# Performance work log

Measured on AMD Instinct MI355X. Metric: run time of the kernel, lower is better.

Reference implementation:

```python
import jax, jax.numpy as jnp
import numpy as np

N_NODES = 50000
N_EDGES = 1600000
IN_CH = 512
OUT_CH = 512

def setup_inputs() -> dict:
    key = jax.random.key(0)
    k1, k2, k3, k4, k5 = jax.random.split(key, 5)
    x = jax.random.normal(k1, (N_NODES, IN_CH), dtype=jnp.float32)
    adj_vals = jax.random.uniform(k2, (N_EDGES,), dtype=jnp.float32)
    edge_row = jax.random.randint(k3, (N_EDGES,), 0, N_NODES, dtype=jnp.int32)
    edge_col = jax.random.randint(k4, (N_EDGES,), 0, N_NODES, dtype=jnp.int32)
    # weight init per reset_parameters: uniform(-stdv, stdv), stdv = 1/sqrt(out_channel)
    stdv = 1.0 / np.sqrt(OUT_CH)
    weight = jax.random.uniform(k5, (IN_CH, OUT_CH), dtype=jnp.float32,
                                minval=-stdv, maxval=stdv)
    return {"x": x, "adj_vals": adj_vals, "edge_row": edge_row,
            "edge_col": edge_col, "weight": weight}

def reference(x, adj_vals, edge_row, edge_col, weight):
    # support = x @ W  -- dense projection [N, out]
    support = x @ weight
    # output = spmm(adj, support): out[i] = sum_j adj[i, j] * support[j]
    # COO: for edge e = (row, col, val), accumulate val * support[col] into out[row]
    msgs = adj_vals[:, None] * support[edge_col]  # [E, out]
    output = jax.ops.segment_sum(msgs, edge_row, num_segments=N_NODES)
    return output
```

## Files before the change

kernel.cpp:

```cpp
#include <hip/hip_runtime.h>
#include <hip/hip_bf16.h>

#define N_NODES 50000
#define N_EDGES 1600000
#define CH 512
#define M_PAD 50048
#define SCAN_B 196

typedef float f32x4 __attribute__((ext_vector_type(4)));
typedef unsigned short ushort8v __attribute__((ext_vector_type(8)));
typedef _Float16 half8v __attribute__((ext_vector_type(8)));

#define GLOAD_LDS16(gptr, lptr)                                                        \
    __builtin_amdgcn_global_load_lds((const __attribute__((address_space(1))) void*)(gptr), \
                                     (__attribute__((address_space(3))) void*)(lptr), 16, 0, 0)

__device__ inline unsigned short f2h(float x) {
    union { _Float16 h; unsigned short u; } cv;
    cv.h = (_Float16)x;
    return cv.u;
}
__device__ inline float h2f(unsigned short u) {
    union { unsigned short u; _Float16 h; } cv;
    cv.u = u;
    return (float)cv.h;
}


__global__ __launch_bounds__(256) void hist_kernel(const int* __restrict__ row,
                                                   int* __restrict__ counts) {
    int e = blockIdx.x * 256 + threadIdx.x;
    if (e < N_EDGES) atomicAdd(&counts[row[e]], 1);
}

__global__ __launch_bounds__(256) void bsum_kernel(const int* __restrict__ counts,
                                                   int* __restrict__ bsum) {
    __shared__ int red[256];
    int i = blockIdx.x * 256 + threadIdx.x;
    red[threadIdx.x] = (i < N_NODES) ? counts[i] : 0;
    __syncthreads();
    for (int s = 128; s > 0; s >>= 1) {
        if (threadIdx.x < s) red[threadIdx.x] += red[threadIdx.x + s];
        __syncthreads();
    }
    if (threadIdx.x == 0) bsum[blockIdx.x] = red[0];
}

__global__ __launch_bounds__(256) void bscan_kernel(const int* __restrict__ bsum,
                                                    int* __restrict__ bbase) {
    __shared__ int sc[256];
    int t = threadIdx.x;
    int v = (t < SCAN_B) ? bsum[t] : 0;
    sc[t] = v;
    __syncthreads();
    for (int d = 1; d < 256; d <<= 1) {
        int a = (t >= d) ? sc[t - d] : 0;
        __syncthreads();
        sc[t] += a;
        __syncthreads();
    }
    if (t < SCAN_B) bbase[t] = sc[t] - v;
}

__global__ __launch_bounds__(256) void offsets_kernel(const int* __restrict__ counts,
                                                      const int* __restrict__ bbase,
                                                      int* __restrict__ offsets,
                                                      int* __restrict__ nxt) {
    __shared__ int sc[256];
    int t = threadIdx.x;
    int i = blockIdx.x * 256 + t;
    int v = (i < N_NODES) ? counts[i] : 0;
    sc[t] = v;
    __syncthreads();
    for (int d = 1; d < 256; d <<= 1) {
        int a = (t >= d) ? sc[t - d] : 0;
        __syncthreads();
        sc[t] += a;
        __syncthreads();
    }
    int off = bbase[blockIdx.x] + sc[t] - v;
    if (i < N_NODES) { offsets[i] = off; nxt[i] = off; }
    if (i == 0) offsets[N_NODES] = N_EDGES;
}

__global__ __launch_bounds__(256) void scatter_kernel(const int* __restrict__ row,
                                                      const int* __restrict__ col,
                                                      const float* __restrict__ val,
                                                      int* __restrict__ nxt,
                                                      int2* __restrict__ ep) {
    int e = blockIdx.x * 256 + threadIdx.x;
    if (e < N_EDGES) {
        int r = row[e];
        int p = atomicAdd(&nxt[r], 1);
        ep[p] = make_int2(col[e], __float_as_int(val[e]));
    }
}


__global__ __launch_bounds__(256) void prep_x(const float* __restrict__ X,
                                              unsigned short* __restrict__ Xa) {
    const int t = threadIdx.x;
    const int m = blockIdx.x * 32 + (t >> 3);
    const int cpart = t & 7;
    float xv[64];
    if (m < N_NODES) {
        const float* xp = &X[(size_t)m * CH + cpart * 64];
#pragma unroll
        for (int i = 0; i < 16; ++i)
            *(float4*)&xv[i * 4] = *(const float4*)&xp[i * 4];
    } else {
#pragma unroll
        for (int i = 0; i < 64; ++i) xv[i] = 0.f;
    }
#pragma unroll
    for (int kk = 0; kk < 2; ++kk) {
        const int kt = cpart * 2 + kk;
        ushort8v o[4];
#pragma unroll
        for (int q = 0; q < 32; ++q)
            o[q >> 3][q & 7] = f2h(xv[kk * 32 + q]);
        unsigned short* dst = &Xa[((size_t)kt * M_PAD + m) * 32];
        *(ushort8v*)&dst[0]  = o[0];
        *(ushort8v*)&dst[8]  = o[1];
        *(ushort8v*)&dst[16] = o[2];
        *(ushort8v*)&dst[24] = o[3];
    }
}


__global__ __launch_bounds__(256) void prep_w(const float* __restrict__ W,
                                              unsigned short* __restrict__ Wb) {
    __shared__ float tile[32][65];
    const int kt = blockIdx.x;
    const int nb = blockIdx.y * 64;
    const int t = threadIdx.x;
    const int nl = t & 63, kl = t >> 6;
#pragma unroll
    for (int p = 0; p < 8; ++p) {
        int k = p * 4 + kl;
        tile[k][nl] = W[(size_t)(kt * 32 + k) * CH + nb + nl];
    }
    __syncthreads();
    const int n_local = t >> 2, j = t & 3;
    ushort8v hi, lo;
#pragma unroll
    for (int q = 0; q < 8; ++q) {
        float x = tile[j * 8 + q][n_local];
        unsigned short h = f2h(x);
        hi[q] = h;
        lo[q] = f2h(x - h2f(h));
    }
    size_t base = ((size_t)kt * 512 + nb + n_local) * 64 + j * 8;
    *(ushort8v*)&Wb[base] = hi;
    *(ushort8v*)&Wb[base + 32] = lo;
}


__global__ __launch_bounds__(256) void gemm_kernel(const unsigned short* __restrict__ Xa,
                                                   const unsigned short* __restrict__ Wb,
                                                   unsigned short* __restrict__ S) {
    __shared__ __align__(16) unsigned short Al[128 * 32];
    __shared__ __align__(16) unsigned short Bl[128 * 64];

    const int tid = threadIdx.x;
    const int wave = tid >> 6;
    const int lane = tid & 63;
    const int wm = (wave >> 1) * 64;
    const int wn = (wave & 1) * 64;
    const int m0 = blockIdx.x * 128;
    const int n0 = blockIdx.y * 128;

    const int lrow = lane >> 3, lslot = lane & 7;
    const int b_lane_off = lrow * 64 + ((lslot ^ lrow) << 3);
    const int arow_l = lane >> 2, aslot = lane & 3;
    const int a_lane_off = arow_l * 32 + ((aslot ^ (arow_l & 3)) << 3);

    const int fr = lane & 15;
    const int fs = lane >> 4;
    const int fx3 = fr & 3;
    const int fx7 = fr & 7;

    f32x4 acc[4][4] = {};

    for (int kt = 0; kt < 16; ++kt) {
        const unsigned short* bsrc = Wb + ((size_t)kt * 512 + n0 + wave * 32) * 64 + b_lane_off;
        unsigned short* bdst = &Bl[(wave * 32) * 64];
        GLOAD_LDS16(bsrc, bdst);
        GLOAD_LDS16(bsrc + 512, bdst + 512);
        GLOAD_LDS16(bsrc + 1024, bdst + 1024);
        GLOAD_LDS16(bsrc + 1536, bdst + 1536);

        const unsigned short* asrc = Xa + ((size_t)kt * M_PAD + m0 + wave * 16) * 32 + a_lane_off;
        unsigned short* adst = &Al[(wave * 16) * 32];
        GLOAD_LDS16(asrc, adst);
        GLOAD_LDS16(asrc + 64 * 32, adst + 64 * 32);

        __syncthreads();

        half8v af[4];
#pragma unroll
        for (int mi = 0; mi < 4; ++mi)
            af[mi] = *(const half8v*)&Al[(wm + mi * 16 + fr) * 32 + ((fs ^ fx3) << 3)];
#pragma unroll
        for (int ni = 0; ni < 4; ++ni) {
            const unsigned short* br = &Bl[(wn + ni * 16 + fr) * 64];
            half8v bhi = *(const half8v*)&br[((fs ^ fx7) << 3)];
            half8v blo = *(const half8v*)&br[(((fs | 4) ^ fx7) << 3)];
#pragma unroll
            for (int mi = 0; mi < 4; ++mi) {
                acc[mi][ni] = __builtin_amdgcn_mfma_f32_16x16x32_f16(af[mi], bhi, acc[mi][ni], 0, 0, 0);
                acc[mi][ni] = __builtin_amdgcn_mfma_f32_16x16x32_f16(af[mi], blo, acc[mi][ni], 0, 0, 0);
            }
        }
        __syncthreads();
    }

    const int crow = (lane >> 4) * 4;
    const int ccol = lane & 15;
#pragma unroll
    for (int mi = 0; mi < 4; ++mi) {
#pragma unroll
        for (int r = 0; r < 4; ++r) {
            int gm = m0 + wm + mi * 16 + crow + r;
            if (gm < N_NODES) {
#pragma unroll
                for (int ni = 0; ni < 4; ++ni) {
                    S[(size_t)gm * CH + n0 + wn + ni * 16 + ccol] = f2h(acc[mi][ni][r]);
                }
            }
        }
    }
}


__global__ __launch_bounds__(128) void spmm_kernel(const int* __restrict__ offsets,
                                                   const int2* __restrict__ ep,
                                                   const unsigned short* __restrict__ S,
                                                   float* __restrict__ out) {
    const int r = blockIdx.x * 2 + (threadIdx.x >> 6);
    const int lane = threadIdx.x & 63;
    const int c = lane * 8;
    const int start = offsets[r];
    const int end = offsets[r + 1];

    float acc[8] = {0.f, 0.f, 0.f, 0.f, 0.f, 0.f, 0.f, 0.f};
    int e = start;
    for (; e + 3 < end; e += 4) {
        const int2 e0 = ep[e];
        const int2 e1 = ep[e + 1];
        const int2 e2 = ep[e + 2];
        const int2 e3 = ep[e + 3];
        const half8v s0 = *(const half8v*)&S[(size_t)e0.x * CH + c];
        const half8v s1 = *(const half8v*)&S[(size_t)e1.x * CH + c];
        const half8v s2 = *(const half8v*)&S[(size_t)e2.x * CH + c];
        const half8v s3 = *(const half8v*)&S[(size_t)e3.x * CH + c];
        const float v0 = __int_as_float(e0.y);
        const float v1 = __int_as_float(e1.y);
        const float v2 = __int_as_float(e2.y);
        const float v3 = __int_as_float(e3.y);
#pragma unroll
        for (int j = 0; j < 8; ++j) {
            acc[j] += v0 * (float)s0[j];
            acc[j] += v1 * (float)s1[j];
            acc[j] += v2 * (float)s2[j];
            acc[j] += v3 * (float)s3[j];
        }
    }
    for (; e < end; ++e) {
        const int2 e0 = ep[e];
        const half8v s0 = *(const half8v*)&S[(size_t)e0.x * CH + c];
        const float v0 = __int_as_float(e0.y);
#pragma unroll
        for (int j = 0; j < 8; ++j) acc[j] += v0 * (float)s0[j];
    }
    float4 o0 = {acc[0], acc[1], acc[2], acc[3]};
    float4 o1 = {acc[4], acc[5], acc[6], acc[7]};
    *(float4*)&out[(size_t)r * CH + c] = o0;
    *(float4*)&out[(size_t)r * CH + c + 4] = o1;
}


extern "C" void kernel_launch(void* const* d_in, const int* in_sizes, int n_in,
                              void* d_out, int out_size, void* d_ws, size_t ws_size,
                              hipStream_t stream) {
    const float* x        = (const float*)d_in[0];
    const float* adj_vals = (const float*)d_in[1];
    const int*   edge_row = (const int*)d_in[2];
    const int*   edge_col = (const int*)d_in[3];
    const float* weight   = (const float*)d_in[4];
    float* out = (float*)d_out;

    auto align256 = [](size_t v) { return (v + 255) & ~(size_t)255; };
    char* ws = (char*)d_ws;
    size_t off = 0;
    unsigned short* support = (unsigned short*)(ws + off); off = align256(off + (size_t)N_NODES * CH * sizeof(unsigned short));
    unsigned short* Xa = (unsigned short*)(ws + off);      off = align256(off + (size_t)16 * M_PAD * 32 * sizeof(unsigned short));
    int*   counts  = (int*)(ws + off);            off = align256(off + (size_t)N_NODES * sizeof(int));
    int*   offsets = (int*)(ws + off);            off = align256(off + (size_t)(N_NODES + 1) * sizeof(int));
    int*   nxt     = (int*)(ws + off);            off = align256(off + (size_t)N_NODES * sizeof(int));
    int2*  ep      = (int2*)(ws + off);           off = align256(off + (size_t)N_EDGES * sizeof(int2));
    unsigned short* Wb = (unsigned short*)(ws + off); off = align256(off + (size_t)16 * 512 * 64 * sizeof(unsigned short));
    int*   bsum    = (int*)(ws + off);            off = align256(off + (size_t)SCAN_B * sizeof(int));
    int*   bbase   = (int*)(ws + off);            off = align256(off + (size_t)SCAN_B * sizeof(int));

    (void)hipMemsetAsync(counts, 0, (size_t)N_NODES * sizeof(int), stream);

    const int EB = (N_EDGES + 255) / 256;
    hist_kernel<<<EB, 256, 0, stream>>>(edge_row, counts);
    bsum_kernel<<<SCAN_B, 256, 0, stream>>>(counts, bsum);
    bscan_kernel<<<1, 256, 0, stream>>>(bsum, bbase);
    offsets_kernel<<<SCAN_B, 256, 0, stream>>>(counts, bbase, offsets, nxt);
    scatter_kernel<<<EB, 256, 0, stream>>>(edge_row, edge_col, adj_vals, nxt, ep);

    prep_x<<<M_PAD / 32, 256, 0, stream>>>(x, Xa);
    dim3 wgrid(16, 8);
    prep_w<<<wgrid, 256, 0, stream>>>(weight, Wb);

    dim3 ggrid(M_PAD / 128, CH / 128);
    gemm_kernel<<<ggrid, 256, 0, stream>>>(Xa, Wb, support);

    spmm_kernel<<<N_NODES / 2, 128, 0, stream>>>(offsets, ep, support, out);
}
```

Measured before the change: 675.8 us.

## Double-buffer GEMM LDS tiles and deepen SpMM gather unroll to eight

The GEMM now keeps two LDS buffers and issues the global-to-LDS loads for the next K tile before computing on the current one. It uses explicit waitcnt and barriers instead of two __syncthreads per iteration, so memory latency can overlap MFMA work. The SpMM inner loop is unrolled from 4 to 8 edges so more independent row gathers are in flight per wave. The cost is twice the LDS per block, which may lower occupancy, and higher register pressure in both kernels.

```diff
diff --git a/kernel.cpp b/kernel.cpp
--- a/kernel.cpp
+++ b/kernel.cpp
@@ -159,8 +159,8 @@
 __global__ __launch_bounds__(256) void gemm_kernel(const unsigned short* __restrict__ Xa,
                                                    const unsigned short* __restrict__ Wb,
                                                    unsigned short* __restrict__ S) {
-    __shared__ __align__(16) unsigned short Al[128 * 32];
-    __shared__ __align__(16) unsigned short Bl[128 * 64];
+    __shared__ __align__(16) unsigned short Al[2][128 * 32];
+    __shared__ __align__(16) unsigned short Bl[2][128 * 64];
 
     const int tid = threadIdx.x;
     const int wave = tid >> 6;
@@ -175,6 +175,9 @@
     const int arow_l = lane >> 2, aslot = lane & 3;
     const int a_lane_off = arow_l * 32 + ((aslot ^ (arow_l & 3)) << 3);
 
+    const unsigned short* bsrc0 = Wb + ((size_t)(n0 + wave * 32)) * 64 + b_lane_off;
+    const unsigned short* asrc0 = Xa + ((size_t)(m0 + wave * 16)) * 32 + a_lane_off;
+
     const int fr = lane & 15;
     const int fs = lane >> 4;
     const int fx3 = fr & 3;
@@ -182,37 +185,59 @@
 
     f32x4 acc[4][4] = {};
 
-    for (int kt = 0; kt < 16; ++kt) {
-        const unsigned short* bsrc = Wb + ((size_t)kt * 512 + n0 + wave * 32) * 64 + b_lane_off;
-        unsigned short* bdst = &Bl[(wave * 32) * 64];
+    {
+        const unsigned short* bsrc = bsrc0;
+        unsigned short* bdst = &Bl[0][(wave * 32) * 64];
         GLOAD_LDS16(bsrc, bdst);
         GLOAD_LDS16(bsrc + 512, bdst + 512);
         GLOAD_LDS16(bsrc + 1024, bdst + 1024);
         GLOAD_LDS16(bsrc + 1536, bdst + 1536);
-
-        const unsigned short* asrc = Xa + ((size_t)kt * M_PAD + m0 + wave * 16) * 32 + a_lane_off;
-        unsigned short* adst = &Al[(wave * 16) * 32];
+        const unsigned short* asrc = asrc0;
+        unsigned short* adst = &Al[0][(wave * 16) * 32];
         GLOAD_LDS16(asrc, adst);
         GLOAD_LDS16(asrc + 64 * 32, adst + 64 * 32);
-
-        __syncthreads();
-
-        half8v af[4];
+    }
+
+#pragma unroll
+    for (int kt = 0; kt < 16; ++kt) {
+        const int cur = kt & 1;
+        asm volatile("s_waitcnt vmcnt(0)" ::: "memory");
+        __builtin_amdgcn_s_barrier();
+
+        if (kt < 15) {
+            const unsigned short* bsrc = bsrc0 + (size_t)(kt + 1) * (512 * 64);
+            unsigned short* bdst = &Bl[cur ^ 1][(wave * 32) * 64];
+            GLOAD_LDS16(bsrc, bdst);
+            GLOAD_LDS16(bsrc + 512, bdst + 512);
+            GLOAD_LDS16(bsrc + 1024, bdst + 1024);
+            GLOAD_LDS16(bsrc + 1536, bdst + 1536);
+            const unsigned short* asrc = asrc0 + (size_t)(kt + 1) * ((size_t)M_PAD * 32);
+            unsigned short* adst = &Al[cur ^ 1][(wave * 16) * 32];
+            GLOAD_LDS16(asrc, adst);
+            GLOAD_LDS16(asrc + 64 * 32, adst + 64 * 32);
+        }
+
+        half8v af[4], bh[4], bl[4];
 #pragma unroll
         for (int mi = 0; mi < 4; ++mi)
-            af[mi] = *(const half8v*)&Al[(wm + mi * 16 + fr) * 32 + ((fs ^ fx3) << 3)];
+            af[mi] = *(const half8v*)&Al[cur][(wm + mi * 16 + fr) * 32 + ((fs ^ fx3) << 3)];
 #pragma unroll
         for (int ni = 0; ni < 4; ++ni) {
-            const unsigned short* br = &Bl[(wn + ni * 16 + fr) * 64];
-            half8v bhi = *(const half8v*)&br[((fs ^ fx7) << 3)];
-            half8v blo = *(const half8v*)&br[(((fs | 4) ^ fx7) << 3)];
+            const unsigned short* br = &Bl[cur][(wn + ni * 16 + fr) * 64];
+            bh[ni] = *(const half8v*)&br[((fs ^ fx7) << 3)];
+            bl[ni] = *(const half8v*)&br[(((fs | 4) ^ fx7) << 3)];
+        }
+        asm volatile("s_waitcnt lgkmcnt(0)" ::: "memory");
+        __builtin_amdgcn_sched_barrier(0);
+        __builtin_amdgcn_s_barrier();
+
+#pragma unroll
+        for (int ni = 0; ni < 4; ++ni)
 #pragma unroll
             for (int mi = 0; mi < 4; ++mi) {
-                acc[mi][ni] = __builtin_amdgcn_mfma_f32_16x16x32_f16(af[mi], bhi, acc[mi][ni], 0, 0, 0);
-                acc[mi][ni] = __builtin_amdgcn_mfma_f32_16x16x32_f16(af[mi], blo, acc[mi][ni], 0, 0, 0);
+                acc[mi][ni] = __builtin_amdgcn_mfma_f32_16x16x32_f16(af[mi], bh[ni], acc[mi][ni], 0, 0, 0);
+                acc[mi][ni] = __builtin_amdgcn_mfma_f32_16x16x32_f16(af[mi], bl[ni], acc[mi][ni], 0, 0, 0);
             }
-        }
-        __syncthreads();
     }
 
     const int crow = (lane >> 4) * 4;
@@ -245,25 +270,19 @@
 
     float acc[8] = {0.f, 0.f, 0.f, 0.f, 0.f, 0.f, 0.f, 0.f};
     int e = start;
-    for (; e + 3 < end; e += 4) {
-        const int2 e0 = ep[e];
-        const int2 e1 = ep[e + 1];
-        const int2 e2 = ep[e + 2];
-        const int2 e3 = ep[e + 3];
-        const half8v s0 = *(const half8v*)&S[(size_t)e0.x * CH + c];
-        const half8v s1 = *(const half8v*)&S[(size_t)e1.x * CH + c];
-        const half8v s2 = *(const half8v*)&S[(size_t)e2.x * CH + c];
-        const half8v s3 = *(const half8v*)&S[(size_t)e3.x * CH + c];
-        const float v0 = __int_as_float(e0.y);
-        const float v1 = __int_as_float(e1.y);
-        const float v2 = __int_as_float(e2.y);
-        const float v3 = __int_as_float(e3.y);
-#pragma unroll
-        for (int j = 0; j < 8; ++j) {
-            acc[j] += v0 * (float)s0[j];
-            acc[j] += v1 * (float)s1[j];
-            acc[j] += v2 * (float)s2[j];
-            acc[j] += v3 * (float)s3[j];
+    for (; e + 7 < end; e += 8) {
+        int2 ee[8];
+#pragma unroll
+        for (int u = 0; u < 8; ++u) ee[u] = ep[e + u];
+        half8v sv[8];
+#pragma unroll
+        for (int u = 0; u < 8; ++u)
+            sv[u] = *(const half8v*)&S[(size_t)ee[u].x * CH + c];
+#pragma unroll
+        for (int u = 0; u < 8; ++u) {
+            const float v = __int_as_float(ee[u].y);
+#pragma unroll
+            for (int j = 0; j < 8; ++j) acc[j] += v * (float)sv[u][j];
         }
     }
     for (; e < end; ++e) {
```

New measurement: 666.5 us. Within noise of the previous version (-1.4%).
